# Kernel tuning notes

Measured on AMD Instinct MI355X. Metric: run time of the kernel, lower is better.

The kernel has to match this reference:

```python
import jax, jax.numpy as jnp
import numpy as np

N, S, H, IN = 512, 128, 512, 2
INF = 1e7  # matches PointerNetAttention.inf


def setup_inputs() -> dict:
    key = jax.random.key(0)
    ks = jax.random.split(key, 12)
    u = lambda k, shp: jax.random.uniform(k, shp, jnp.float32, -0.08, 0.08)
    return {
        "x": jax.random.normal(ks[0], (N, S, IN), jnp.float32),
        "r": jax.random.normal(ks[1], (N, S, H), jnp.float32),
        "h0": jax.random.normal(ks[2], (1, N, H), jnp.float32) * 0.1,
        "c0": jax.random.normal(ks[3], (1, N, H), jnp.float32) * 0.1,
        # LSTM (num_layers=1), PyTorch layout: gates ordered i,f,g,o
        "W_ih": u(ks[4], (4 * H, IN)),
        "W_hh": u(ks[5], (4 * H, H)),
        "b_ih": u(ks[6], (4 * H,)),
        "b_hh": u(ks[7], (4 * H,)),
        # pointer attention params
        "w_ref": u(ks[8], (1, H, H)),
        "w_q": u(ks[9], (H, H)),
        "v": u(ks[10], (1, H)),
        "bos": u(ks[11], (1, 1, IN)),
    }


def reference(x, r, h0, c0, W_ih, W_hh, b_ih, b_hh, w_ref, w_q, v, bos):
    n, s, _ = r.shape
    # precompute encoder projection r @ w_ref once (loop-invariant)
    rW = jnp.einsum('nsh,hk->nsk', r, w_ref[0])
    init = (h0[0], c0[0],
            jnp.broadcast_to(bos[0, 0], (n, x.shape[2])),  # prev node = BOS
            jnp.zeros((n, s), r.dtype),                    # visited mask
            jnp.zeros((n,), r.dtype))                      # log-likelihood

    def step(carry, _):
        h, c, prev, mask, ll = carry
        # single-layer LSTM cell (seq len 1 per step)
        gates = prev @ W_ih.T + h @ W_hh.T + b_ih + b_hh
        i, f, g, o = jnp.split(gates, 4, axis=-1)
        c_new = jax.nn.sigmoid(f) * c + jax.nn.sigmoid(i) * jnp.tanh(g)
        h_new = jax.nn.sigmoid(o) * jnp.tanh(c_new)
        # pointer attention score
        q = h_new @ w_q
        score = jnp.einsum('nsh,h->ns', jnp.tanh(rW + q[:, None, :]), v[0]) - INF * mask
        logp = jax.nn.log_softmax(score, axis=1)
        pos = jnp.argmax(logp, axis=1)  # greedy selection
        ll = ll + jnp.take_along_axis(logp, pos[:, None], axis=1)[:, 0]
        mask = jnp.maximum(mask, jax.nn.one_hot(pos, s, dtype=mask.dtype))
        prev_new = jnp.take_along_axis(x, pos[:, None, None], axis=1)[:, 0, :]
        return (h_new, c_new, prev_new, mask, ll), pos

    (_, _, _, _, ll), tour = jax.lax.scan(step, init, None, length=s)
    return tour.T, ll  # pred_tour [N, S] (int), log_ll [N]
```

## Files before the change

kernel.cpp:

```cpp
#include <hip/hip_runtime.h>
#include <math.h>


namespace {
constexpr int NB  = 512;
constexpr int S   = 128;
constexpr int H   = 512;
constexpr int G   = 4;
constexpr int NBLK = NB / G;
constexpr float INFV = 1e7f;

__device__ __forceinline__ float ftanh(float x) {
  x = fminf(fmaxf(x, -15.f), 15.f);
  return 1.f - 2.f * __builtin_amdgcn_rcpf(__expf(2.f * x) + 1.f);
}
__device__ __forceinline__ float fsigm(float x) {
  x = fminf(fmaxf(x, -30.f), 30.f);
  return __builtin_amdgcn_rcpf(1.f + __expf(-x));
}
}

__global__ __launch_bounds__(256) void k_pack(const float* __restrict__ Whh,
                                              const float* __restrict__ wq,
                                              float* __restrict__ whhp,
                                              float* __restrict__ wqp) {
  int i = blockIdx.x * 256 + threadIdx.x;
  if (i < 2048 * 512) {
    int m = i >> 9, k = i & 511;
    whhp[(size_t)(k >> 2) * 8192 + m * 4 + (k & 3)] = Whh[i];
  }
  int j2 = i - 2048 * 512;
  if (j2 >= 0 && j2 < 512 * 512) {
    int k = j2 >> 9, j = j2 & 511;
    wqp[(size_t)(k >> 2) * 2048 + j * 4 + (k & 3)] = wq[j2];
  }
}

__global__ __launch_bounds__(256) void k_rw(const float* __restrict__ r,
                                            const float* __restrict__ wref,
                                            float* __restrict__ rW) {
  __shared__ float As[16][64];
  __shared__ float Bs[16][64];
  const int tid = threadIdx.x;
  const int tx = tid & 15, ty = tid >> 4;
  const int M0 = blockIdx.x * 64, N0 = blockIdx.y * 64;
  float acc[4][4] = {};
  for (int k0 = 0; k0 < H; k0 += 16) {
    {
      int row = tid >> 2, c4 = (tid & 3) * 4;
      float4 a = *(const float4*)&r[(size_t)(M0 + row) * H + k0 + c4];
      As[c4+0][row] = a.x; As[c4+1][row] = a.y; As[c4+2][row] = a.z; As[c4+3][row] = a.w;
    }
    {
      int row = tid >> 4, c4 = (tid & 15) * 4;
      *(float4*)&Bs[row][c4] = *(const float4*)&wref[(size_t)(k0 + row) * H + N0 + c4];
    }
    __syncthreads();
#pragma unroll
    for (int kk = 0; kk < 16; ++kk) {
      float4 a = *(float4*)&As[kk][ty*4];
      float4 b = *(float4*)&Bs[kk][tx*4];
      float av[4] = {a.x,a.y,a.z,a.w}, bv[4] = {b.x,b.y,b.z,b.w};
#pragma unroll
      for (int i = 0; i < 4; ++i)
#pragma unroll
        for (int j = 0; j < 4; ++j) acc[i][j] += av[i]*bv[j];
    }
    __syncthreads();
  }
#pragma unroll
  for (int i = 0; i < 4; ++i)
    *(float4*)&rW[(size_t)(M0 + ty*4 + i) * H + N0 + tx*4] =
        make_float4(acc[i][0], acc[i][1], acc[i][2], acc[i][3]);
}

struct DecArgs {
  const float *x, *h0, *c0, *Wih, *bih, *bhh, *v, *bos;
  const float *whhp, *wqp, *rW;
  float *out_tour, *out_ll;
};

__global__ __launch_bounds__(512) void k_decode(DecArgs a) {
  const int tid  = threadIdx.x;
  const int b    = blockIdx.x;
  const int n0   = b * G;
  const int lane = tid & 63, wave = tid >> 6;

  __shared__ float h_[2][G][H];
  __shared__ float c_[G][H];
  __shared__ float q_[G][H];
  __shared__ float ms_[G][S];
  __shared__ float sc_[G][S];
  __shared__ float prev_[G][2];
  __shared__ float ll_[G];

  for (int i = tid; i < G * H; i += 512) {
    int n = i >> 9, k = i & 511;
    h_[0][n][k] = a.h0[(size_t)(n0 + n) * H + k];
    c_[n][k]    = a.c0[(size_t)(n0 + n) * H + k];
  }
  for (int i = tid; i < G * S; i += 512) ms_[i >> 7][i & 127] = 0.f;
  if (tid < G) {
    ll_[tid] = 0.f;
    prev_[tid][0] = a.bos[0];
    prev_[tid][1] = a.bos[1];
  }

  float bsum[4], wi0[4], wi1[4];
#pragma unroll
  for (int g = 0; g < 4; ++g) {
    int m = g * H + tid;
    bsum[g] = a.bih[m] + a.bhh[m];
    wi0[g]  = a.Wih[2 * m];
    wi1[g]  = a.Wih[2 * m + 1];
  }
  const float4 vA = *(const float4*)&a.v[lane * 8];
  const float4 vB = *(const float4*)&a.v[lane * 8 + 4];
  __syncthreads();

  for (int t = 0; t < S; ++t) {
    const int cur = t & 1, nxt = cur ^ 1;

    {
      float acc[G][4] = {};
#pragma unroll 2
      for (int k4 = 0; k4 < 128; ++k4) {
        float4 h4[G];
#pragma unroll
        for (int n = 0; n < G; ++n) h4[n] = *(const float4*)&h_[cur][n][k4 * 4];
        const float* wp = &a.whhp[(size_t)k4 * 8192 + tid * 4];
#pragma unroll
        for (int g = 0; g < 4; ++g) {
          float4 w4 = *(const float4*)&wp[g * 2048];
#pragma unroll
          for (int n = 0; n < G; ++n)
            acc[n][g] += h4[n].x * w4.x + h4[n].y * w4.y
                       + h4[n].z * w4.z + h4[n].w * w4.w;
        }
      }
#pragma unroll
      for (int n = 0; n < G; ++n) {
        float p0 = prev_[n][0], p1 = prev_[n][1];
        float gv[4];
#pragma unroll
        for (int g = 0; g < 4; ++g)
          gv[g] = acc[n][g] + bsum[g] + p0 * wi0[g] + p1 * wi1[g];
        float cv = c_[n][tid];
        float cn = fsigm(gv[1]) * cv + fsigm(gv[0]) * ftanh(gv[2]);
        float hn = fsigm(gv[3]) * ftanh(cn);
        c_[n][tid] = cn;
        h_[nxt][n][tid] = hn;
      }
    }
    __syncthreads();

    {
      float accq[G] = {};
#pragma unroll 4
      for (int k4 = 0; k4 < 128; ++k4) {
        float4 w4 = *(const float4*)&a.wqp[(size_t)k4 * 2048 + tid * 4];
#pragma unroll
        for (int n = 0; n < G; ++n) {
          float4 h4 = *(const float4*)&h_[nxt][n][k4 * 4];
          accq[n] += h4.x * w4.x + h4.y * w4.y + h4.z * w4.z + h4.w * w4.w;
        }
      }
#pragma unroll
      for (int n = 0; n < G; ++n) q_[n][tid] = accq[n];
    }
    __syncthreads();

    {
      const int n  = wave >> 1;
      const int s0 = (wave & 1) * 64;
      const float4 qA = *(const float4*)&q_[n][lane * 8];
      const float4 qB = *(const float4*)&q_[n][lane * 8 + 4];
      const float* rwn = a.rW + ((size_t)(n0 + n) * S + s0) * H + lane * 8;
#pragma unroll 1
      for (int bq = 0; bq < 8; ++bq) {
        float4 A0[8], A1[8];
#pragma unroll
        for (int rr = 0; rr < 8; ++rr) {
          const float* rp = rwn + (size_t)(bq * 8 + rr) * H;
          A0[rr] = *(const float4*)rp;
          A1[rr] = *(const float4*)(rp + 4);
        }
#pragma unroll
        for (int rr = 0; rr < 8; ++rr) {
          float sr = ftanh(A0[rr].x + qA.x) * vA.x + ftanh(A0[rr].y + qA.y) * vA.y
                   + ftanh(A0[rr].z + qA.z) * vA.z + ftanh(A0[rr].w + qA.w) * vA.w
                   + ftanh(A1[rr].x + qB.x) * vB.x + ftanh(A1[rr].y + qB.y) * vB.y
                   + ftanh(A1[rr].z + qB.z) * vB.z + ftanh(A1[rr].w + qB.w) * vB.w;
#pragma unroll
          for (int off = 32; off > 0; off >>= 1) sr += __shfl_down(sr, off);
          if (lane == 0) {
            int s = s0 + bq * 8 + rr;
            sc_[n][s] = sr - INFV * ms_[n][s];
          }
        }
      }
    }
    __syncthreads();
    if (wave < G) {
      const int n = wave;
      float v0 = sc_[n][lane], v1 = sc_[n][lane + 64];
      float bv; int bi;
      if (v1 > v0) { bv = v1; bi = lane + 64; } else { bv = v0; bi = lane; }
#pragma unroll
      for (int off = 32; off > 0; off >>= 1) {
        float ov = __shfl_down(bv, off);
        int   oi = __shfl_down(bi, off);
        if (ov > bv || (ov == bv && oi < bi)) { bv = ov; bi = oi; }
      }
      bv = __shfl(bv, 0); bi = __shfl(bi, 0);
      float e = __expf(sc_[n][lane] - bv) + __expf(sc_[n][lane + 64] - bv);
#pragma unroll
      for (int off = 32; off > 0; off >>= 1) e += __shfl_down(e, off);
      if (lane == 0) {
        float nll = ll_[n] - logf(e);
        ll_[n] = nll;
        a.out_ll[n0 + n] = nll;
        a.out_tour[(size_t)(n0 + n) * S + t] = (float)bi;
        ms_[n][bi] = 1.f;
        prev_[n][0] = a.x[((size_t)(n0 + n) * S + bi) * 2 + 0];
        prev_[n][1] = a.x[((size_t)(n0 + n) * S + bi) * 2 + 1];
      }
    }
    __syncthreads();
  }
}

extern "C" void kernel_launch(void* const* d_in, const int* in_sizes, int n_in,
                              void* d_out, int out_size, void* d_ws, size_t ws_size,
                              hipStream_t stream) {
  const float* x    = (const float*)d_in[0];
  const float* r    = (const float*)d_in[1];
  const float* h0   = (const float*)d_in[2];
  const float* c0   = (const float*)d_in[3];
  const float* Wih  = (const float*)d_in[4];
  const float* Whh  = (const float*)d_in[5];
  const float* bih  = (const float*)d_in[6];
  const float* bhh  = (const float*)d_in[7];
  const float* wref = (const float*)d_in[8];
  const float* wq   = (const float*)d_in[9];
  const float* v    = (const float*)d_in[10];
  const float* bos  = (const float*)d_in[11];
  float* out = (float*)d_out;
  float* ws  = (float*)d_ws;

  size_t off = 0;
  float* rW   = ws + off; off += (size_t)NB * S * H;
  float* whhp = ws + off; off += (size_t)4 * H * H;
  float* wqp  = ws + off; off += (size_t)H * H;

  k_pack<<<(2048*512 + 512*512 + 255) / 256, 256, 0, stream>>>(Whh, wq, whhp, wqp);
  k_rw<<<dim3(NB * S / 64, H / 64), 256, 0, stream>>>(r, wref, rW);

  DecArgs da;
  da.x = x; da.h0 = h0; da.c0 = c0; da.Wih = Wih; da.bih = bih; da.bhh = bhh;
  da.v = v; da.bos = bos; da.whhp = whhp; da.wqp = wqp; da.rW = rW;
  da.out_tour = out; da.out_ll = out + (size_t)NB * S;

  k_decode<<<NBLK, 512, 0, stream>>>(da);
}
```

Before: 14.01 ms.

## Score only unvisited nodes and align blocks with a global step barrier

The attention scoring stage now keeps a per-row compact list of unvisited nodes (swap-remove with an inverse index), so only alive rows of rW are loaded and pass through tanh. Argmax and softmax iterate only over alive entries, replacing the -INF mask. This roughly halves the rW traffic and transcendental work over the tour. A device-wide spin barrier is also added at each step so that all blocks stay in lockstep and share Whh/wq reads in cache, at the cost of a global synchronisation per step and a possible hang if blocks are not co-resident.

```diff
diff --git a/kernel.cpp b/kernel.cpp
--- a/kernel.cpp
+++ b/kernel.cpp
@@ -8,7 +8,6 @@
 constexpr int H   = 512;
 constexpr int G   = 4;
 constexpr int NBLK = NB / G;
-constexpr float INFV = 1e7f;
 
 __device__ __forceinline__ float ftanh(float x) {
   x = fminf(fmaxf(x, -15.f), 15.f);
@@ -18,7 +17,21 @@
   x = fminf(fmaxf(x, -30.f), 30.f);
   return __builtin_amdgcn_rcpf(1.f + __expf(-x));
 }
-}
+
+__device__ __forceinline__ void align_bar(int* bar, int target) {
+  __syncthreads();
+  if (threadIdx.x == 0) {
+    __hip_atomic_fetch_add(bar, 1, __ATOMIC_RELAXED, __HIP_MEMORY_SCOPE_AGENT);
+    int it = 0;
+    while (__hip_atomic_load(bar, __ATOMIC_RELAXED, __HIP_MEMORY_SCOPE_AGENT) < target
+           && ++it < (1 << 20))
+      __builtin_amdgcn_s_sleep(2);
+  }
+  __syncthreads();
+}
+}
+
+__global__ void k_zero(int* bar) { if (threadIdx.x == 0) *bar = 0; }
 
 __global__ __launch_bounds__(256) void k_pack(const float* __restrict__ Whh,
                                               const float* __restrict__ wq,
@@ -78,6 +91,7 @@
   const float *x, *h0, *c0, *Wih, *bih, *bhh, *v, *bos;
   const float *whhp, *wqp, *rW;
   float *out_tour, *out_ll;
+  int *bar;
 };
 
 __global__ __launch_bounds__(512) void k_decode(DecArgs a) {
@@ -89,8 +103,10 @@
   __shared__ float h_[2][G][H];
   __shared__ float c_[G][H];
   __shared__ float q_[G][H];
-  __shared__ float ms_[G][S];
   __shared__ float sc_[G][S];
+  __shared__ unsigned short alive_[G][S];
+  __shared__ unsigned short inv_[G][S];
+  __shared__ int   cnt_[G];
   __shared__ float prev_[G][2];
   __shared__ float ll_[G];
 
@@ -99,8 +115,12 @@
     h_[0][n][k] = a.h0[(size_t)(n0 + n) * H + k];
     c_[n][k]    = a.c0[(size_t)(n0 + n) * H + k];
   }
-  for (int i = tid; i < G * S; i += 512) ms_[i >> 7][i & 127] = 0.f;
+  for (int i = tid; i < G * S; i += 512) {
+    alive_[i >> 7][i & 127] = (unsigned short)(i & 127);
+    inv_[i >> 7][i & 127]   = (unsigned short)(i & 127);
+  }
   if (tid < G) {
+    cnt_[tid] = S;
     ll_[tid] = 0.f;
     prev_[tid][0] = a.bos[0];
     prev_[tid][1] = a.bos[1];
@@ -119,6 +139,8 @@
   __syncthreads();
 
   for (int t = 0; t < S; ++t) {
+    align_bar(a.bar, (t + 1) * NBLK);
+
     const int cur = t & 1, nxt = cur ^ 1;
 
     {
@@ -171,17 +193,24 @@
     __syncthreads();
 
     {
-      const int n  = wave >> 1;
-      const int s0 = (wave & 1) * 64;
+      const int n    = wave >> 1;
+      const int half = wave & 1;
+      const int cnt  = cnt_[n];
       const float4 qA = *(const float4*)&q_[n][lane * 8];
       const float4 qB = *(const float4*)&q_[n][lane * 8 + 4];
-      const float* rwn = a.rW + ((size_t)(n0 + n) * S + s0) * H + lane * 8;
+      const float* rwn = a.rW + (size_t)(n0 + n) * S * H + lane * 8;
 #pragma unroll 1
-      for (int bq = 0; bq < 8; ++bq) {
+      for (int c0 = half * 8; c0 < cnt; c0 += 16) {
+        int rows[8];
         float4 A0[8], A1[8];
 #pragma unroll
         for (int rr = 0; rr < 8; ++rr) {
-          const float* rp = rwn + (size_t)(bq * 8 + rr) * H;
+          int idx = c0 + rr; if (idx > cnt - 1) idx = cnt - 1;
+          rows[rr] = alive_[n][idx];
+        }
+#pragma unroll
+        for (int rr = 0; rr < 8; ++rr) {
+          const float* rp = rwn + (size_t)rows[rr] * H;
           A0[rr] = *(const float4*)rp;
           A1[rr] = *(const float4*)(rp + 4);
         }
@@ -193,19 +222,21 @@
                    + ftanh(A1[rr].z + qB.z) * vB.z + ftanh(A1[rr].w + qB.w) * vB.w;
 #pragma unroll
           for (int off = 32; off > 0; off >>= 1) sr += __shfl_down(sr, off);
-          if (lane == 0) {
-            int s = s0 + bq * 8 + rr;
-            sc_[n][s] = sr - INFV * ms_[n][s];
-          }
-        }
-      }
-    }
-    __syncthreads();
+          if (lane == 0) sc_[n][rows[rr]] = sr;
+        }
+      }
+    }
+    __syncthreads();
+
     if (wave < G) {
       const int n = wave;
-      float v0 = sc_[n][lane], v1 = sc_[n][lane + 64];
-      float bv; int bi;
-      if (v1 > v0) { bv = v1; bi = lane + 64; } else { bv = v0; bi = lane; }
+      const int cnt = cnt_[n];
+      float bv = -3.4e38f; int bi = 1 << 30;
+      for (int i = lane; i < cnt; i += 64) {
+        int s = alive_[n][i];
+        float vv = sc_[n][s];
+        if (vv > bv || (vv == bv && s < bi)) { bv = vv; bi = s; }
+      }
 #pragma unroll
       for (int off = 32; off > 0; off >>= 1) {
         float ov = __shfl_down(bv, off);
@@ -213,7 +244,11 @@
         if (ov > bv || (ov == bv && oi < bi)) { bv = ov; bi = oi; }
       }
       bv = __shfl(bv, 0); bi = __shfl(bi, 0);
-      float e = __expf(sc_[n][lane] - bv) + __expf(sc_[n][lane + 64] - bv);
+      float e = 0.f;
+      for (int i = lane; i < cnt; i += 64) {
+        int s = alive_[n][i];
+        e += __expf(sc_[n][s] - bv);
+      }
 #pragma unroll
       for (int off = 32; off > 0; off >>= 1) e += __shfl_down(e, off);
       if (lane == 0) {
@@ -221,7 +256,11 @@
         ll_[n] = nll;
         a.out_ll[n0 + n] = nll;
         a.out_tour[(size_t)(n0 + n) * S + t] = (float)bi;
-        ms_[n][bi] = 1.f;
+        int p = inv_[n][bi];
+        unsigned short last = alive_[n][cnt - 1];
+        alive_[n][p] = last;
+        inv_[n][last] = (unsigned short)p;
+        cnt_[n] = cnt - 1;
         prev_[n][0] = a.x[((size_t)(n0 + n) * S + bi) * 2 + 0];
         prev_[n][1] = a.x[((size_t)(n0 + n) * S + bi) * 2 + 1];
       }
@@ -252,7 +291,9 @@
   float* rW   = ws + off; off += (size_t)NB * S * H;
   float* whhp = ws + off; off += (size_t)4 * H * H;
   float* wqp  = ws + off; off += (size_t)H * H;
-
+  int*   bar  = (int*)(ws + off); off += 16;
+
+  k_zero<<<1, 64, 0, stream>>>(bar);
   k_pack<<<(2048*512 + 512*512 + 255) / 256, 256, 0, stream>>>(Whh, wq, whhp, wqp);
   k_rw<<<dim3(NB * S / 64, H / 64), 256, 0, stream>>>(r, wref, rW);
 
@@ -260,6 +301,7 @@
   da.x = x; da.h0 = h0; da.c0 = c0; da.Wih = Wih; da.bih = bih; da.bhh = bhh;
   da.v = v; da.bos = bos; da.whhp = whhp; da.wqp = wqp; da.rW = rW;
   da.out_tour = out; da.out_ll = out + (size_t)NB * S;
+  da.bar = bar;
 
   k_decode<<<NBLK, 512, 0, stream>>>(da);
 }
```

Measured after the change: 13.27 ms. -5.3%, faster.
